# Kernel tuning notes

Hardware: AMD Instinct MI355X
Metric: run time of the kernel (lower is better)

The kernel has to match this reference:

```python
import jax, jax.numpy as jnp
import numpy as np

K = 9  # ATSS top-k candidates per GT


def cxcywh_to_xyxy(b):
    cx, cy, w, h = b[..., 0], b[..., 1], b[..., 2], b[..., 3]
    return jnp.stack([cx - 0.5 * w, cy - 0.5 * h, cx + 0.5 * w, cy + 0.5 * h], axis=-1)


def elementwise_iou(a, b):
    # a, b: [..., 4] xyxy, broadcastable
    lt = jnp.maximum(a[..., :2], b[..., :2])
    rb = jnp.minimum(a[..., 2:], b[..., 2:])
    wh = jnp.clip(rb - lt, 0.0)
    inter = wh[..., 0] * wh[..., 1]
    area_a = (a[..., 2] - a[..., 0]) * (a[..., 3] - a[..., 1])
    area_b = (b[..., 2] - b[..., 0]) * (b[..., 3] - b[..., 1])
    return inter / (area_a + area_b - inter)


def setup_inputs() -> dict:
    key = jax.random.key(0)
    k1, k2 = jax.random.split(key)
    pred_boxes = jax.random.uniform(k1, (16, 30000, 4), dtype=jnp.float32)
    gt_boxes = jax.random.uniform(k2, (16, 64, 4), dtype=jnp.float32)
    return {"pred_boxes": pred_boxes, "gt_boxes": gt_boxes}


def reference(pred_boxes, gt_boxes):
    # pred_boxes: [B, N, 4] cxcywh; gt_boxes: [B, G, 4] cxcywh
    G = gt_boxes.shape[1]

    def per_image(pred, gt):
        # center-distance matrix [G, N] (the cdist in the original)
        diff = gt[:, None, :2] - pred[None, :, :2]
        dist = jnp.sqrt(jnp.sum(diff * diff, axis=-1))
        # k smallest distances per GT
        _, k_idx = jax.lax.top_k(-dist, K)          # [G, K]
        k_boxes = pred[k_idx]                        # [G, K, 4]
        gt_xyxy = cxcywh_to_xyxy(gt)                 # [G, 4]
        kb_xyxy = cxcywh_to_xyxy(k_boxes)            # [G, K, 4]
        ious = elementwise_iou(gt_xyxy[:, None, :], kb_xyxy)  # [G, K]
        # adaptive threshold: mean + std (torch.std is unbiased -> ddof=1)
        thr = jnp.mean(ious, axis=1, keepdims=True) + jnp.std(ious, axis=1, ddof=1, keepdims=True)
        cx, cy = k_boxes[..., 0], k_boxes[..., 1]
        inside = ((gt_xyxy[:, None, 0] <= cx) & (cx <= gt_xyxy[:, None, 2]) &
                  (gt_xyxy[:, None, 1] <= cy) & (cy <= gt_xyxy[:, None, 3]))
        mask = (ious >= thr) & inside                # [G, K]
        # padded index representation (original returns ragged lists):
        pred_idx = jnp.where(mask, k_idx, -1)
        gt_idx = jnp.where(mask, jnp.arange(G, dtype=jnp.int64)[:, None], -1)
        return pred_idx, gt_idx, mask, ious

    return jax.vmap(per_image)(pred_boxes, gt_boxes)
```

## Files before the change

kernel.cpp:

```cpp
#include <hip/hip_runtime.h>
#include <stdint.h>

typedef unsigned long long u64;

#define KCAND 9
#define BATCH 16
#define NPRED 30000
#define NGT   64
#define TPB   256
#define INITKEY 0x7F800000FFFFFFFFULL

__device__ __forceinline__ u64 wave_min_u64(u64 v) {
#pragma unroll
    for (int s = 1; s < 64; s <<= 1) {
        u64 o = __shfl_xor(v, s, 64);
        v = o < v ? o : v;
    }
    return v;
}

__global__ __launch_bounds__(TPB, 4) void atss_kernel(
    const float* __restrict__ pred,
    const float* __restrict__ gt,
    float* __restrict__ out)
{
#pragma clang fp contract(off)
    const int tid  = threadIdx.x;
    const int lane = tid & 63;
    const int wvid = tid >> 6;
    const int w    = blockIdx.x;
    const int b    = w >> 6;
    const int g    = w & 63;

    const float4 gtb = ((const float4*)gt)[w];
    const float gcx = gtb.x, gcy = gtb.y;
    const float2* p2    = (const float2*)(pred + (size_t)b * NPRED * 4);
    const float4* pred4 = (const float4*)pred + (size_t)b * NPRED;

    u64 val = INITKEY;
    float Tf = __uint_as_float(0x7F800000u);

    for (int t = 0; t < 30; ++t) {
        const int i0 = t * 1024 + wvid * 256 + lane;
        float d2[4]; int ii[4];
#pragma unroll
        for (int j = 0; j < 4; ++j) {
            const int i = i0 + j * 64;
            ii[j] = i;
            const bool v = i < NPRED;
            const int ic = v ? i : 0;
            float2 xy = p2[2 * ic];
            float dx = __fsub_rn(gcx, xy.x);
            float dy = __fsub_rn(gcy, xy.y);
            float d = __fadd_rn(__fmul_rn(dx, dx), __fmul_rn(dy, dy));
            d2[j] = v ? d : __uint_as_float(0x7F800000u);
        }
        float dmin = fminf(fminf(d2[0], d2[1]), fminf(d2[2], d2[3]));
        if (__ballot(dmin <= Tf) == 0ULL) continue;

#pragma unroll
        for (int j = 0; j < 4; ++j) {
            u64 pend = __ballot(d2[j] <= Tf);
            while (pend) {
                const int src = __ffsll(pend) - 1;
                pend &= pend - 1;
                const unsigned kd = __shfl(__float_as_uint(d2[j]), src, 64);
                const unsigned ki = (unsigned)__shfl(ii[j], src, 64);
                const u64 key = ((u64)kd << 32) | ki;
                u64 Tkey = __shfl(val, 8, 64);
                if (key < Tkey) {
                    const u64 ltm = __ballot(val < key) & 0x1FFULL;
                    const int pos = __popcll(ltm);
                    const u64 sh = __shfl_up(val, 1, 64);
                    if (lane < KCAND) {
                        if (lane == pos)      val = key;
                        else if (lane > pos)  val = sh;
                    }
                    Tkey = __shfl(val, 8, 64);
                    Tf = __uint_as_float((unsigned)(Tkey >> 32));
                    pend &= __ballot(d2[j] <= Tf);
                }
            }
        }
    }

    __shared__ u64 smem[4 * KCAND];
    if (lane < KCAND) smem[wvid * KCAND + lane] = val;
    __syncthreads();

    if (wvid != 0) return;

    u64 key = (lane < 4 * KCAND) ? smem[lane] : ~0ULL;
    u64 fin = 0;
#pragma unroll
    for (int k = 0; k < KCAND; ++k) {
        u64 m = wave_min_u64(key);
        if (lane == k) fin = m;
        if (key == m) key = ~0ULL;
    }

    const bool active = (lane < KCAND);
    const unsigned idx = active ? (unsigned)(fin & 0xffffffffu) : 0u;

    float4 pb = pred4[idx];

    float gx1 = gcx - 0.5f * gtb.z, gy1 = gcy - 0.5f * gtb.w;
    float gx2 = gcx + 0.5f * gtb.z, gy2 = gcy + 0.5f * gtb.w;
    float kx1 = pb.x - 0.5f * pb.z, ky1 = pb.y - 0.5f * pb.w;
    float kx2 = pb.x + 0.5f * pb.z, ky2 = pb.y + 0.5f * pb.w;

    float ltx = fmaxf(gx1, kx1), lty = fmaxf(gy1, ky1);
    float rbx = fminf(gx2, kx2), rby = fminf(gy2, ky2);
    float wvd = fmaxf(rbx - ltx, 0.0f);
    float hvd = fmaxf(rby - lty, 0.0f);
    float inter  = wvd * hvd;
    float area_a = (gx2 - gx1) * (gy2 - gy1);
    float area_b = (kx2 - kx1) * (ky2 - ky1);
    float iou = inter / ((area_a + area_b) - inter);

    float v = active ? iou : 0.0f;
    float s = v;
#pragma unroll
    for (int m = 1; m < 64; m <<= 1) s += __shfl_xor(s, m, 64);
    float mean = s / 9.0f;

    float dev = active ? (iou - mean) : 0.0f;
    float ss = dev * dev;
#pragma unroll
    for (int m = 1; m < 64; m <<= 1) ss += __shfl_xor(ss, m, 64);
    float stdv = sqrtf(ss / 8.0f);
    float thr = mean + stdv;

    bool inside = (gx1 <= pb.x) && (pb.x <= gx2) &&
                  (gy1 <= pb.y) && (pb.y <= gy2);
    bool maskk = (iou >= thr) && inside;

    if (active) {
        const size_t chunk = (size_t)BATCH * NGT * KCAND;
        const size_t o = (size_t)w * KCAND + lane;
        out[0 * chunk + o] = maskk ? (float)idx : -1.0f;
        out[1 * chunk + o] = maskk ? (float)g   : -1.0f;
        out[2 * chunk + o] = maskk ? 1.0f : 0.0f;
        out[3 * chunk + o] = iou;
    }
}

extern "C" void kernel_launch(void* const* d_in, const int* in_sizes, int n_in,
                              void* d_out, int out_size, void* d_ws, size_t ws_size,
                              hipStream_t stream) {
    const float* pred = (const float*)d_in[0];
    const float* gtb  = (const float*)d_in[1];
    float* out = (float*)d_out;

    atss_kernel<<<BATCH * NGT, TPB, 0, stream>>>(pred, gtb, out);
}
```

Measured before the change: 98.20 us.

## Compact box centers into workspace, unroll scan by 8, remap blocks for L2 locality

Adds a pre-pass kernel that writes only the (cx, cy) pairs into a contiguous workspace buffer, so the distance scan reads dense float2 data instead of strided halves of float4 boxes. The scan unroll goes from 4 to 8 with half as many outer iterations. The candidate index is recomputed from the lane instead of shuffled. Block indices are remapped so that concurrently running blocks spread across 8 images. The cost is an extra kernel launch and a full pass over the prediction array; when the workspace is too small the kernel falls back to the strided read.

```diff
diff --git a/kernel.cpp b/kernel.cpp
--- a/kernel.cpp
+++ b/kernel.cpp
@@ -8,6 +8,8 @@
 #define NPRED 30000
 #define NGT   64
 #define TPB   256
+#define UNR   8
+#define NT    15
 #define INITKEY 0x7F800000FFFFFFFFULL
 
 __device__ __forceinline__ u64 wave_min_u64(u64 v) {
@@ -19,53 +21,66 @@
     return v;
 }
 
+__global__ __launch_bounds__(256) void compact_xy(
+    const float* __restrict__ pred, float2* __restrict__ xy)
+{
+    int e = blockIdx.x * 256 + threadIdx.x;
+    if (e < BATCH * NPRED) {
+        float4 p = ((const float4*)pred)[e];
+        xy[e] = make_float2(p.x, p.y);
+    }
+}
+
+template <int S2>
 __global__ __launch_bounds__(TPB, 4) void atss_kernel(
-    const float* __restrict__ pred,
-    const float* __restrict__ gt,
+    const float2* __restrict__ xy,
+    const float*  __restrict__ pred,
+    const float*  __restrict__ gt,
     float* __restrict__ out)
 {
 #pragma clang fp contract(off)
     const int tid  = threadIdx.x;
     const int lane = tid & 63;
     const int wvid = tid >> 6;
-    const int w    = blockIdx.x;
-    const int b    = w >> 6;
-    const int g    = w & 63;
+
+    const int b = (blockIdx.x & 7) + 8 * (blockIdx.x >> 9);
+    const int g = (blockIdx.x >> 3) & 63;
+    const int w = b * NGT + g;
 
     const float4 gtb = ((const float4*)gt)[w];
     const float gcx = gtb.x, gcy = gtb.y;
-    const float2* p2    = (const float2*)(pred + (size_t)b * NPRED * 4);
+    const float2* xyb   = xy + (size_t)b * NPRED * S2;
     const float4* pred4 = (const float4*)pred + (size_t)b * NPRED;
 
     u64 val = INITKEY;
     float Tf = __uint_as_float(0x7F800000u);
 
-    for (int t = 0; t < 30; ++t) {
-        const int i0 = t * 1024 + wvid * 256 + lane;
-        float d2[4]; int ii[4];
+    for (int t = 0; t < NT; ++t) {
+        const int i0 = t * (TPB * UNR) + wvid * (64 * UNR) + lane;
+        float d2[UNR];
 #pragma unroll
-        for (int j = 0; j < 4; ++j) {
+        for (int j = 0; j < UNR; ++j) {
             const int i = i0 + j * 64;
-            ii[j] = i;
             const bool v = i < NPRED;
-            const int ic = v ? i : 0;
-            float2 xy = p2[2 * ic];
-            float dx = __fsub_rn(gcx, xy.x);
-            float dy = __fsub_rn(gcy, xy.y);
+            float2 p = xyb[(v ? i : 0) * S2];
+            float dx = __fsub_rn(gcx, p.x);
+            float dy = __fsub_rn(gcy, p.y);
             float d = __fadd_rn(__fmul_rn(dx, dx), __fmul_rn(dy, dy));
             d2[j] = v ? d : __uint_as_float(0x7F800000u);
         }
-        float dmin = fminf(fminf(d2[0], d2[1]), fminf(d2[2], d2[3]));
+        float dmin = d2[0];
+#pragma unroll
+        for (int j = 1; j < UNR; ++j) dmin = fminf(dmin, d2[j]);
         if (__ballot(dmin <= Tf) == 0ULL) continue;
 
 #pragma unroll
-        for (int j = 0; j < 4; ++j) {
+        for (int j = 0; j < UNR; ++j) {
             u64 pend = __ballot(d2[j] <= Tf);
             while (pend) {
                 const int src = __ffsll(pend) - 1;
                 pend &= pend - 1;
                 const unsigned kd = __shfl(__float_as_uint(d2[j]), src, 64);
-                const unsigned ki = (unsigned)__shfl(ii[j], src, 64);
+                const unsigned ki = (unsigned)(i0 + j * 64 - lane + src);
                 const u64 key = ((u64)kd << 32) | ki;
                 u64 Tkey = __shfl(val, 8, 64);
                 if (key < Tkey) {
@@ -152,5 +167,13 @@
     const float* gtb  = (const float*)d_in[1];
     float* out = (float*)d_out;
 
-    atss_kernel<<<BATCH * NGT, TPB, 0, stream>>>(pred, gtb, out);
+    const size_t need = (size_t)BATCH * NPRED * sizeof(float2);
+    if (ws_size >= need) {
+        float2* xy = (float2*)d_ws;
+        compact_xy<<<(BATCH * NPRED + 255) / 256, 256, 0, stream>>>(pred, xy);
+        atss_kernel<1><<<BATCH * NGT, TPB, 0, stream>>>(xy, pred, gtb, out);
+    } else {
+        atss_kernel<2><<<BATCH * NGT, TPB, 0, stream>>>(
+            (const float2*)pred, pred, gtb, out);
+    }
 }
```

New measurement: 97.49 us. No clear change (-0.7%).
